# Performance work log

Measured on AMD Instinct MI355X. Metric: run time of the kernel, lower is better.

The kernel has to match this reference:

```python
import jax, jax.numpy as jnp
import numpy as np

D_MODEL = 2048
EXPAND = 2
D_INNER = EXPAND * D_MODEL      # 4096
HEADDIM = 64
NHEADS = D_INNER // HEADDIM     # 64
D_STATE = 128
NGROUPS = 1
D_CONV = 4
CHUNK = 256
CONV_DIM = D_INNER + 2 * NGROUPS * D_STATE          # 4352
D_IN_PROJ = 2 * D_INNER + 2 * NGROUPS * D_STATE + NHEADS  # 8512
EPS = 1e-5


def setup_inputs() -> dict:
    key = jax.random.key(0)
    ks = jax.random.split(key, 8)
    B, L = 2, 2048
    u = jax.random.normal(ks[0], (B, L, D_MODEL), jnp.float32)
    W_in = jax.random.normal(ks[1], (D_IN_PROJ, D_MODEL), jnp.float32) / np.sqrt(D_MODEL)
    conv_w = jax.random.normal(ks[2], (CONV_DIM, D_CONV), jnp.float32) * 0.2
    conv_b = jax.random.normal(ks[3], (CONV_DIM,), jnp.float32) * 0.05
    # dt_bias initialized exactly as in the torch module
    dt = jnp.exp(jax.random.uniform(ks[4], (NHEADS,)) * (np.log(0.1) - np.log(0.001)) + np.log(0.001))
    dt = jnp.clip(dt, 1e-4)
    dt_bias = dt + jnp.log(-jnp.expm1(-dt))
    A_log = jnp.log(jax.random.uniform(ks[5], (NHEADS,), minval=1.0, maxval=16.0))
    D = jnp.ones((NHEADS,), jnp.float32)
    norm_w = jnp.ones((D_INNER,), jnp.float32)
    W_out = jax.random.normal(ks[6], (D_MODEL, D_INNER), jnp.float32) / np.sqrt(D_INNER)
    return dict(u=u, W_in=W_in, conv_w=conv_w, conv_b=conv_b, dt_bias=dt_bias,
                A_log=A_log, D=D, norm_w=norm_w, W_out=W_out)


def _segsum(x):
    # x: (..., l) -> (..., l, l) with out[i, j] = sum_{k=j+1..i} x[k] (lower-tri, -inf above)
    cs = jnp.cumsum(x, -1)
    seg = cs[..., :, None] - cs[..., None, :]
    l = x.shape[-1]
    mask = jnp.tril(jnp.ones((l, l), bool))
    return jnp.where(mask, seg, -jnp.inf)


def reference(u, W_in, conv_w, conv_b, dt_bias, A_log, D, norm_w, W_out):
    B, L, _ = u.shape
    zxbcdt = u @ W_in.T                                   # (B, L, 8512)
    z, xBC, dt_raw = jnp.split(zxbcdt, [D_INNER, D_INNER + CONV_DIM], axis=-1)
    # depthwise causal conv1d + SiLU (padding = d_conv-1, truncated to seqlen)
    xpad = jnp.pad(xBC, ((0, 0), (D_CONV - 1, 0), (0, 0)))
    xconv = conv_b + sum(xpad[:, w:w + L, :] * conv_w[:, w] for w in range(D_CONV))
    xBC = jax.nn.silu(xconv)
    x, Bm, Cm = jnp.split(xBC, [D_INNER, D_INNER + NGROUPS * D_STATE], axis=-1)
    x = x.reshape(B, L, NHEADS, HEADDIM)
    hpg = NHEADS // NGROUPS
    Bh = jnp.repeat(Bm.reshape(B, L, NGROUPS, D_STATE), hpg, axis=2)  # (B,L,H,N)
    Ch = jnp.repeat(Cm.reshape(B, L, NGROUPS, D_STATE), hpg, axis=2)
    dt = jax.nn.softplus(dt_raw + dt_bias)                # (B, L, H)
    A = -jnp.exp(A_log)                                   # (H,)
    nchunks = L // CHUNK
    def chunk(t):
        return t.reshape(B, nchunks, CHUNK, *t.shape[2:])
    xc, Bc, Cc, dtc = chunk(x), chunk(Bh), chunk(Ch), chunk(dt)
    xd = xc * dtc[..., None]                              # (B,C,Lc,H,P)
    dA = jnp.transpose(dtc * A, (0, 3, 1, 2))             # (B,H,C,Lc)
    A_cum = jnp.cumsum(dA, -1)
    Lmat = jnp.exp(_segsum(dA))                           # (B,H,C,Lc,Lc) lower-tri decays
    # intra-chunk (diagonal blocks)
    Y_diag = jnp.einsum('bclhn,bcshn,bhcls,bcshp->bclhp', Cc, Bc, Lmat, xd)
    # chunk end-states
    decay_states = jnp.exp(A_cum[..., -1:] - A_cum)       # (B,H,C,Lc)
    states = jnp.einsum('bclhn,bhcl,bclhp->bchpn', Bc, decay_states, xd)
    # inter-chunk recurrence over chunk states
    chunk_sums = jnp.pad(A_cum[..., -1], ((0, 0), (0, 0), (1, 0)))  # (B,H,C+1)
    decay_chunk = jnp.exp(_segsum(chunk_sums))            # (B,H,C+1,C+1)
    states_pad = jnp.concatenate([jnp.zeros_like(states[:, :1]), states], axis=1)
    new_states = jnp.einsum('bhzc,bchpn->bzhpn', decay_chunk, states_pad)
    prev_states = new_states[:, :-1]                      # (B,C,H,P,N)
    Y_off = jnp.einsum('bclhn,bchpn,bhcl->bclhp', Cc, prev_states, jnp.exp(A_cum))
    y = (Y_diag + Y_off).reshape(B, L, NHEADS, HEADDIM)
    y = y + x * D[None, None, :, None]                    # per-head D skip
    y = y.reshape(B, L, D_INNER)
    # gated RMSNorm (norm_before_gate=False): rmsnorm(y * silu(z)) * w
    yg = y * jax.nn.silu(z)
    var = jnp.mean(yg * yg, axis=-1, keepdims=True)
    y = yg * jax.lax.rsqrt(var + EPS) * norm_w
    return y @ W_out.T                                    # (B, L, d_model)
```

## Files before the change

kernel.cpp:

```cpp
#include <hip/hip_runtime.h>

#define D_MODEL   2048
#define D_INNER   4096
#define HEADDIM   64
#define NHEADS    64
#define D_STATE   128
#define CHUNK     256
#define CONV_DIM  4352
#define D_IN_PROJ 8512
#define BATCH     2
#define SEQ       2048
#define NCHUNK    8
#define NROWS     4096
#define EPSV      1e-5f
#define CG        (CONV_DIM / 8)

typedef __attribute__((ext_vector_type(8))) short bf16x8;
typedef __attribute__((ext_vector_type(8))) unsigned short u16x8;
typedef __attribute__((ext_vector_type(4))) float f32x4;

#define AS1 __attribute__((address_space(1)))
#define AS3 __attribute__((address_space(3)))

#define BAR() do { asm volatile("" ::: "memory"); __builtin_amdgcn_s_barrier(); asm volatile("" ::: "memory"); } while (0)

__device__ __forceinline__ unsigned short f2bf(float f) {
  unsigned int x = __float_as_uint(f);
  unsigned int r = (x + 0x7fffu + ((x >> 16) & 1u)) >> 16;
  return (unsigned short)r;
}
__device__ __forceinline__ float bf2f(unsigned short u) {
  return __uint_as_float((unsigned int)u << 16);
}

__global__ void k_sentinel(float* out) { if (threadIdx.x == 0) out[0] = 1.0e6f; }

__global__ void k_f32_to_bf16_v4(const float* __restrict__ in, unsigned short* __restrict__ out, long n4) {
  long i = (long)blockIdx.x * blockDim.x + threadIdx.x;
  long stride = (long)gridDim.x * blockDim.x;
  for (; i < n4; i += stride) {
    float4 v = ((const float4*)in)[i];
    ushort4 o = make_ushort4(f2bf(v.x), f2bf(v.y), f2bf(v.z), f2bf(v.w));
    ((ushort4*)out)[i] = o;
  }
}

__global__ void k_usplit(const float* __restrict__ in, unsigned short* __restrict__ hi,
                         unsigned short* __restrict__ lo, long n4) {
  long i = (long)blockIdx.x * blockDim.x + threadIdx.x;
  long stride = (long)gridDim.x * blockDim.x;
  for (; i < n4; i += stride) {
    float4 v = ((const float4*)in)[i];
    ushort4 h, l;
    h.x = f2bf(v.x); l.x = f2bf(v.x - bf2f(h.x));
    h.y = f2bf(v.y); l.y = f2bf(v.y - bf2f(h.y));
    h.z = f2bf(v.z); l.z = f2bf(v.z - bf2f(h.z));
    h.w = f2bf(v.w); l.w = f2bf(v.w - bf2f(h.w));
    ((ushort4*)hi)[i] = h;
    ((ushort4*)lo)[i] = l;
  }
}

__global__ void k_wpack(const float* __restrict__ W, unsigned short* __restrict__ whl) {
  long i = (long)blockIdx.x * blockDim.x + threadIdx.x;
  if (i >= (long)64 * D_MODEL) return;
  float v = W[(size_t)8448 * D_MODEL + i];
  unsigned short h = f2bf(v);
  whl[i] = h;
  whl[(size_t)64 * D_MODEL + i] = f2bf(v - bf2f(h));
}

__global__ __launch_bounds__(256, 2) void k_dtm(const unsigned short* __restrict__ uhi,
                                                const unsigned short* __restrict__ ulo,
                                                const unsigned short* __restrict__ whl,
                                                float* __restrict__ PD) {
  __shared__ __align__(16) short lds[2][256 * 64];
  const int t = threadIdx.x;
  const int lane = t & 63;
  const int w = t >> 6;
  const int ks = (int)blockIdx.x & 3;
  const int m0 = ((int)blockIdx.x >> 2) * 64;
  const int kbase = ks * 512;

  f32x4 acc1[8], acc2[4];
#pragma unroll
  for (int j = 0; j < 8; ++j) { f32x4 z = {0.f, 0.f, 0.f, 0.f}; acc1[j] = z; }
#pragma unroll
  for (int j = 0; j < 4; ++j) { f32x4 z = {0.f, 0.f, 0.f, 0.f}; acc2[j] = z; }

  const int srow = t >> 3;
  const int schunk = (t & 7) ^ (srow & 7);
  const unsigned short* gU = uhi + (size_t)(m0 + srow) * D_MODEL + kbase + schunk * 8;
  const unsigned short* gL = ulo + (size_t)(m0 + srow) * D_MODEL + kbase + schunk * 8;
  const unsigned short* gW = whl + (size_t)srow * D_MODEL + kbase + schunk * 8;

  auto STAGE = [&](int buf, int kt) {
    char* d = (char*)&lds[buf][0] + t * 16;
#pragma unroll
    for (int ii = 0; ii < 2; ++ii)
      __builtin_amdgcn_global_load_lds((const AS1 void*)(gU + (size_t)ii * 32 * D_MODEL + (size_t)kt * 64),
                                       (AS3 void*)(d + ii * 4096), 16, 0, 0);
#pragma unroll
    for (int ii = 0; ii < 2; ++ii)
      __builtin_amdgcn_global_load_lds((const AS1 void*)(gL + (size_t)ii * 32 * D_MODEL + (size_t)kt * 64),
                                       (AS3 void*)(d + 8192 + ii * 4096), 16, 0, 0);
#pragma unroll
    for (int ii = 0; ii < 4; ++ii)
      __builtin_amdgcn_global_load_lds((const AS1 void*)(gW + (size_t)ii * 32 * D_MODEL + (size_t)kt * 64),
                                       (AS3 void*)(d + 16384 + ii * 4096), 16, 0, 0);
  };

  STAGE(0, 0);

  const int NT = 512 / 64;
  const int ar = w * 16 + (lane & 15);
  const int kof = (lane >> 4) * 8;
  const int rsw = (lane & 7) * 8;
  int cur = 0;
  for (int kt = 0; kt < NT; ++kt) {
    if (kt + 1 < NT) {
      STAGE(cur ^ 1, kt + 1);
      asm volatile("s_waitcnt vmcnt(8)" ::: "memory");
    } else {
      asm volatile("s_waitcnt vmcnt(0)" ::: "memory");
    }
    __builtin_amdgcn_s_barrier();
    asm volatile("" ::: "memory");
    const short* L = &lds[cur][0];
#pragma unroll
    for (int kk = 0; kk < 2; ++kk) {
      const int off = (kk * 32 + kof) ^ rsw;
      bf16x8 ah = *(const bf16x8*)(L + ar * 64 + off);
      bf16x8 al = *(const bf16x8*)(L + (64 + ar) * 64 + off);
#pragma unroll
      for (int j = 0; j < 8; ++j) {
        bf16x8 bj = *(const bf16x8*)(L + (128 + j * 16 + (lane & 15)) * 64 + off);
        acc1[j] = __builtin_amdgcn_mfma_f32_16x16x32_bf16(ah, bj, acc1[j], 0, 0, 0);
        if (j < 4) acc2[j] = __builtin_amdgcn_mfma_f32_16x16x32_bf16(al, bj, acc2[j], 0, 0, 0);
      }
    }
    asm volatile("" ::: "memory");
    __builtin_amdgcn_s_barrier();
    asm volatile("" ::: "memory");
    cur ^= 1;
  }

  const int crow = (lane >> 4) * 4;
  float* P = PD + (size_t)ks * BATCH * NHEADS * SEQ;
#pragma unroll
  for (int j = 0; j < 4; ++j) {
    int h = j * 16 + (lane & 15);
#pragma unroll
    for (int r = 0; r < 4; ++r) {
      int row = m0 + w * 16 + crow + r;
      float v = acc1[j][r] + acc1[j + 4][r] + acc2[j][r];
      P[(size_t)((row >> 11) * NHEADS + h) * SEQ + (row & 2047)] = v;
    }
  }
}

__global__ __launch_bounds__(256) void k_dtred(const float* __restrict__ PD, const float* __restrict__ dt_bias,
                                               const float* __restrict__ A_log,
                                               float* __restrict__ dt_t, float* __restrict__ A_cum) {
  const int bh = blockIdx.x;
  const int h = bh & 63;
  const int t = threadIdx.x;
  const float bias = dt_bias[h];
  const float A = -expf(A_log[h]);
  const size_t base = (size_t)bh * SEQ;
  const size_t pstride = (size_t)BATCH * NHEADS * SEQ;
  __shared__ float s[256];
  for (int c = 0; c < NCHUNK; ++c) {
    int l = c * CHUNK + t;
    float v = PD[base + l] + PD[pstride + base + l] + PD[2 * pstride + base + l] + PD[3 * pstride + base + l] + bias;
    float dtv = (v > 20.f) ? v : log1pf(expf(v));
    dt_t[base + l] = dtv;
    s[t] = dtv * A;
    __syncthreads();
    for (int off = 1; off < 256; off <<= 1) {
      float x = (t >= off) ? s[t - off] : 0.f;
      __syncthreads();
      s[t] += x;
      __syncthreads();
    }
    A_cum[((size_t)bh * NCHUNK + c) * CHUNK + t] = s[t];
    __syncthreads();
  }
}

__global__ __launch_bounds__(512, 2) void k_gemm8p(const unsigned short* __restrict__ A,
                                                   const unsigned short* __restrict__ B,
                                                   unsigned short* __restrict__ C, int M, int N, int K) {
  __shared__ __align__(16) short lds[2][32768];
  const int t = threadIdx.x;
  const int lane = t & 63;
  const int wid = t >> 6;
  const int wr = wid >> 2;
  const int wc = wid & 3;
  const int ntx = N / 256;
  const int nwg = (int)gridDim.x;
  const int bid = (int)blockIdx.x;
  const int swzb = (bid & 7) * (nwg >> 3) + (bid >> 3);
  const int m0 = (swzb / ntx) * 256;
  const int n0 = (swzb % ntx) * 256;

  f32x4 acc[8][4];
#pragma unroll
  for (int i = 0; i < 8; ++i)
#pragma unroll
    for (int j = 0; j < 4; ++j) { f32x4 z = {0.f, 0.f, 0.f, 0.f}; acc[i][j] = z; }

  const int srow = t >> 3;
  const int schunk = (t & 7) ^ (srow & 7);
  const unsigned short* gA = A + (size_t)(m0 + srow) * K + schunk * 8;
  const unsigned short* gB = B + (size_t)(n0 + srow) * K + schunk * 8;

  auto STAGE_HALF = [&](int buf, int kt, int which) {
    const unsigned short* g = (which < 2 ? gA : gB) + (size_t)(which & 1) * 128 * K + (size_t)kt * 64;
    char* d = (char*)lds + buf * 65536 + which * 16384 + t * 16;
    __builtin_amdgcn_global_load_lds((const AS1 void*)g, (AS3 void*)d, 16, 0, 0);
    __builtin_amdgcn_global_load_lds((const AS1 void*)(g + (size_t)64 * K), (AS3 void*)(d + 8192), 16, 0, 0);
  };

  const int NT = K / 64;
  STAGE_HALF(0, 0, 0); STAGE_HALF(0, 0, 1); STAGE_HALF(0, 0, 2); STAGE_HALF(0, 0, 3);
  STAGE_HALF(1, 1, 2); STAGE_HALF(1, 1, 0); STAGE_HALF(1, 1, 1);
  asm volatile("s_waitcnt vmcnt(6)" ::: "memory");
  BAR();

  const int ar = wr * 128 + (lane & 15);
  const int br = wc * 64 + (lane & 15);
  const int kof = (lane >> 4) * 8;
  const int rsw = (lane & 7) * 8;

  for (int kt = 0; kt < NT; ++kt) {
    const int buf = kt & 1;
    const short* As = &lds[buf][0];
    const short* Bs = &lds[buf][16384];
    const bool s1 = (kt + 1 < NT);
    const bool s2 = (kt + 2 < NT);
    bf16x8 aLo[4][2], aHi[4][2], bLo[2][2], bHi[2][2];

#pragma unroll
    for (int i = 0; i < 4; ++i)
#pragma unroll
      for (int k = 0; k < 2; ++k) aLo[i][k] = *(const bf16x8*)(As + (ar + i * 16) * 64 + ((k * 32 + kof) ^ rsw));
#pragma unroll
    for (int j = 0; j < 2; ++j)
#pragma unroll
      for (int k = 0; k < 2; ++k) bLo[j][k] = *(const bf16x8*)(Bs + (br + j * 16) * 64 + ((k * 32 + kof) ^ rsw));
    if (s1) STAGE_HALF(buf ^ 1, kt + 1, 3);
    BAR();
    __builtin_amdgcn_s_setprio(1);
#pragma unroll
    for (int k = 0; k < 2; ++k)
#pragma unroll
      for (int i = 0; i < 4; ++i)
#pragma unroll
        for (int j = 0; j < 2; ++j)
          acc[i][j] = __builtin_amdgcn_mfma_f32_16x16x32_bf16(aLo[i][k], bLo[j][k], acc[i][j], 0, 0, 0);
    __builtin_amdgcn_s_setprio(0);
    BAR();

#pragma unroll
    for (int j = 0; j < 2; ++j)
#pragma unroll
      for (int k = 0; k < 2; ++k) bHi[j][k] = *(const bf16x8*)(Bs + (br + (j + 2) * 16) * 64 + ((k * 32 + kof) ^ rsw));
    BAR();
    __builtin_amdgcn_s_setprio(1);
#pragma unroll
    for (int k = 0; k < 2; ++k)
#pragma unroll
      for (int i = 0; i < 4; ++i)
#pragma unroll
        for (int j = 0; j < 2; ++j)
          acc[i][j + 2] = __builtin_amdgcn_mfma_f32_16x16x32_bf16(aLo[i][k], bHi[j][k], acc[i][j + 2], 0, 0, 0);
    __builtin_amdgcn_s_setprio(0);
    BAR();

#pragma unroll
    for (int i = 0; i < 4; ++i)
#pragma unroll
      for (int k = 0; k < 2; ++k) aHi[i][k] = *(const bf16x8*)(As + (ar + (i + 4) * 16) * 64 + ((k * 32 + kof) ^ rsw));
    if (s2) STAGE_HALF(buf, kt + 2, 2);
    BAR();
    __builtin_amdgcn_s_setprio(1);
#pragma unroll
    for (int k = 0; k < 2; ++k)
#pragma unroll
      for (int i = 0; i < 4; ++i)
#pragma unroll
        for (int j = 0; j < 2; ++j)
          acc[i + 4][j] = __builtin_amdgcn_mfma_f32_16x16x32_bf16(aHi[i][k], bLo[j][k], acc[i + 4][j], 0, 0, 0);
    __builtin_amdgcn_s_setprio(0);
    BAR();

    if (s2) { STAGE_HALF(buf, kt + 2, 0); STAGE_HALF(buf, kt + 2, 1); }
    if (s2) { asm volatile("s_waitcnt vmcnt(6)" ::: "memory"); }
    else    { asm volatile("s_waitcnt vmcnt(0)" ::: "memory"); }
    BAR();
    __builtin_amdgcn_s_setprio(1);
#pragma unroll
    for (int k = 0; k < 2; ++k)
#pragma unroll
      for (int i = 0; i < 4; ++i)
#pragma unroll
        for (int j = 0; j < 2; ++j)
          acc[i + 4][j + 2] = __builtin_amdgcn_mfma_f32_16x16x32_bf16(aHi[i][k], bHi[j][k], acc[i + 4][j + 2], 0, 0, 0);
    __builtin_amdgcn_s_setprio(0);
    BAR();
  }

  const int crow = (lane >> 4) * 4;
  const int ccol = lane & 15;
#pragma unroll
  for (int i = 0; i < 8; ++i)
#pragma unroll
    for (int j = 0; j < 4; ++j) {
      size_t base = (size_t)(m0 + wr * 128 + i * 16 + crow) * N + (n0 + wc * 64 + j * 16 + ccol);
#pragma unroll
      for (int r = 0; r < 4; ++r) C[base + (size_t)r * N] = f2bf(acc[i][j][r]);
    }
}

template <int BF16OUT>
__global__ __launch_bounds__(256, 2) void k_gemm128(const unsigned short* __restrict__ A,
                                                    const unsigned short* __restrict__ B,
                                                    void* __restrict__ Cv, int M, int N, int K) {
  constexpr int BK = 64;
  __shared__ __align__(16) short lds[2][256 * BK];
  const int t = threadIdx.x;
  const int lane = t & 63;
  const int wid = t >> 6;
  const int wr = wid >> 1;
  const int wc = wid & 1;
  const int ntx = N / 128;
  const int nwg = (int)gridDim.x;
  const int bid = (int)blockIdx.x;
  const int swzb = (bid & 7) * (nwg >> 3) + (bid >> 3);
  const int m0 = (swzb / ntx) * 128;
  const int n0 = (swzb % ntx) * 128;

  f32x4 acc[4][4];
#pragma unroll
  for (int i = 0; i < 4; ++i)
#pragma unroll
    for (int j = 0; j < 4; ++j) { f32x4 z = {0.f, 0.f, 0.f, 0.f}; acc[i][j] = z; }

  const int srow = t >> 3;
  const int schunk = (t & 7) ^ (srow & 7);
  const unsigned short* gA = A + (size_t)(m0 + srow) * K + schunk * 8;
  const unsigned short* gB = B + (size_t)(n0 + srow) * K + schunk * 8;

  auto STAGE = [&](int buf, int kt) {
    char* dA = (char*)&lds[buf][0] + t * 16;
    char* dB = (char*)&lds[buf][128 * BK] + t * 16;
#pragma unroll
    for (int ii = 0; ii < 4; ++ii)
      __builtin_amdgcn_global_load_lds((const AS1 void*)(gA + (size_t)ii * 32 * K + kt * BK),
                                       (AS3 void*)(dA + ii * 4096), 16, 0, 0);
#pragma unroll
    for (int ii = 0; ii < 4; ++ii)
      __builtin_amdgcn_global_load_lds((const AS1 void*)(gB + (size_t)ii * 32 * K + kt * BK),
                                       (AS3 void*)(dB + ii * 4096), 16, 0, 0);
  };

  STAGE(0, 0);

  const int NT = K / BK;
  const int ar = wr * 64 + (lane & 15);
  const int br = wc * 64 + (lane & 15);
  const int kof = (lane >> 4) * 8;
  const int rsw = (lane & 7) * 8;
  int cur = 0;
  for (int kt = 0; kt < NT; ++kt) {
    if (kt + 1 < NT) {
      STAGE(cur ^ 1, kt + 1);
      asm volatile("s_waitcnt vmcnt(8)" ::: "memory");
    } else {
      asm volatile("s_waitcnt vmcnt(0)" ::: "memory");
    }
    __builtin_amdgcn_s_barrier();
    asm volatile("" ::: "memory");
    const short* As = &lds[cur][0];
    const short* Bs = &lds[cur][128 * BK];
#pragma unroll
    for (int kk = 0; kk < 2; ++kk) {
      bf16x8 bfr[4];
#pragma unroll
      for (int j = 0; j < 4; ++j)
        bfr[j] = *(const bf16x8*)(Bs + (br + j * 16) * BK + ((kk * 32 + kof) ^ rsw));
#pragma unroll
      for (int i = 0; i < 4; ++i) {
        bf16x8 af = *(const bf16x8*)(As + (ar + i * 16) * BK + ((kk * 32 + kof) ^ rsw));
#pragma unroll
        for (int j = 0; j < 4; ++j)
          acc[i][j] = __builtin_amdgcn_mfma_f32_16x16x32_bf16(af, bfr[j], acc[i][j], 0, 0, 0);
      }
    }
    asm volatile("" ::: "memory");
    __builtin_amdgcn_s_barrier();
    asm volatile("" ::: "memory");
    cur ^= 1;
  }

  const int crow = (lane >> 4) * 4;
  const int ccol = lane & 15;
#pragma unroll
  for (int i = 0; i < 4; ++i)
#pragma unroll
    for (int j = 0; j < 4; ++j) {
      size_t base = (size_t)(m0 + wr * 64 + i * 16 + crow) * N + (n0 + wc * 64 + j * 16 + ccol);
      if (BF16OUT) {
        unsigned short* C = (unsigned short*)Cv;
#pragma unroll
        for (int r = 0; r < 4; ++r) C[base + (size_t)r * N] = f2bf(acc[i][j][r]);
      } else {
        float* C = (float*)Cv;
#pragma unroll
        for (int r = 0; r < 4; ++r) C[base + (size_t)r * N] = acc[i][j][r];
      }
    }
}

__global__ void k_conv_pack(const float* __restrict__ cw, const float* __restrict__ cb,
                            unsigned short* __restrict__ wT, unsigned short* __restrict__ bT) {
  int i = blockIdx.x * blockDim.x + threadIdx.x;
  if (i < CONV_DIM) {
#pragma unroll
    for (int w = 0; w < 4; ++w) wT[w * CONV_DIM + i] = f2bf(cw[i * 4 + w]);
    bT[i] = f2bf(cb[i]);
  }
}

__global__ __launch_bounds__(256) void k_conv_silu(const unsigned short* __restrict__ xb,
                                                   const unsigned short* __restrict__ wT,
                                                   const unsigned short* __restrict__ bT,
                                                   unsigned short* __restrict__ out) {
  long idx = (long)blockIdx.x * blockDim.x + threadIdx.x;
  if (idx >= (long)(NROWS / 4) * CG) return;
  int c8 = (int)(idx % CG);
  long rq = idx / CG;
  int l0 = (int)((rq & (SEQ / 4 - 1)) * 4);
  long brow = (rq >> 9) * (long)SEQ;
  int ch0 = c8 * 8;

  u16x8 wv[4];
#pragma unroll
  for (int w = 0; w < 4; ++w) wv[w] = *(const u16x8*)(wT + w * CONV_DIM + ch0);
  u16x8 bv = *(const u16x8*)(bT + ch0);

  u16x8 xr[7];
#pragma unroll
  for (int i = 0; i < 7; ++i) {
    int ls = l0 - 3 + i;
    if (ls >= 0) xr[i] = *(const u16x8*)(xb + (brow + ls) * (long)CONV_DIM + ch0);
    else { u16x8 z = {0, 0, 0, 0, 0, 0, 0, 0}; xr[i] = z; }
  }

#pragma unroll
  for (int r = 0; r < 4; ++r) {
    float acc[8];
#pragma unroll
    for (int e = 0; e < 8; ++e) acc[e] = bf2f(bv[e]);
#pragma unroll
    for (int w = 0; w < 4; ++w)
#pragma unroll
      for (int e = 0; e < 8; ++e) acc[e] += bf2f(xr[r + w][e]) * bf2f(wv[w][e]);
    u16x8 o;
#pragma unroll
    for (int e = 0; e < 8; ++e) o[e] = f2bf(acc[e] / (1.f + expf(-acc[e])));
    *(u16x8*)(out + (brow + l0 + r) * (long)CONV_DIM + ch0) = o;
  }
}

__global__ __launch_bounds__(256) void k_cbtt(const unsigned short* __restrict__ xbc, unsigned short* __restrict__ cbt_t) {
  const int bid = blockIdx.x;
  const int sp = bid & 3;
  const int bc = bid >> 2;
  const int b = bc >> 3, c = bc & 7;
  const int t = threadIdx.x;
  const int lane = t & 63;
  const int w = t >> 6;
  const int g = lane >> 4;
  __shared__ unsigned short Cs[256][72];
  __shared__ unsigned short Bs2[64][72];
  const long rowbase = (long)b * SEQ + c * CHUNK;
  f32x4 acc[4][4];
#pragma unroll
  for (int i = 0; i < 4; ++i)
#pragma unroll
    for (int j = 0; j < 4; ++j) { f32x4 z = {0.f, 0.f, 0.f, 0.f}; acc[i][j] = z; }

  for (int np = 0; np < 2; ++np) {
    __syncthreads();
    for (int i = t; i < 256 * 16; i += 256) {
      int row = i >> 4, c4 = (i & 15) * 4;
      ushort4 v = *(const ushort4*)(xbc + (rowbase + row) * (long)CONV_DIM + D_INNER + D_STATE + np * 64 + c4);
      *(ushort4*)&Cs[row][c4] = v;
    }
    for (int i = t; i < 64 * 16; i += 256) {
      int row = i >> 4, c4 = (i & 15) * 4;
      ushort4 v = *(const ushort4*)(xbc + (rowbase + sp * 64 + row) * (long)CONV_DIM + D_INNER + np * 64 + c4);
      *(ushort4*)&Bs2[row][c4] = v;
    }
    __syncthreads();
#pragma unroll
    for (int ks = 0; ks < 2; ++ks) {
      const int kofs = ks * 32 + g * 8;
      bf16x8 af[4], bfr[4];
#pragma unroll
      for (int i = 0; i < 4; ++i) af[i] = *(const bf16x8*)&Cs[w * 64 + i * 16 + (lane & 15)][kofs];
#pragma unroll
      for (int j = 0; j < 4; ++j) bfr[j] = *(const bf16x8*)&Bs2[j * 16 + (lane & 15)][kofs];
#pragma unroll
      for (int i = 0; i < 4; ++i)
#pragma unroll
        for (int j = 0; j < 4; ++j)
          acc[i][j] = __builtin_amdgcn_mfma_f32_16x16x32_bf16(af[i], bfr[j], acc[i][j], 0, 0, 0);
    }
  }
  unsigned short* ob = cbt_t + (long)bc * CHUNK * CHUNK;
#pragma unroll
  for (int i = 0; i < 4; ++i)
#pragma unroll
    for (int j = 0; j < 4; ++j) {
      int l0 = w * 64 + i * 16 + g * 4;
      int s = sp * 64 + j * 16 + (lane & 15);
#pragma unroll
      for (int r = 0; r < 4; ++r) ob[(long)(l0 + r) * CHUNK + s] = f2bf(acc[i][j][r]);
    }
}

__global__ __launch_bounds__(256) void k_states(const unsigned short* __restrict__ xbc, const float* __restrict__ dt_t,
                                                const float* __restrict__ A_cum, float* __restrict__ states) {
  const int bid = blockIdx.x;
  const int h = bid & 63;
  const int bc = bid >> 6;
  const int b = bc >> 3, c = bc & 7;
  const int t = threadIdx.x;
  const int lane = t & 63;
  const int w = t >> 6;
  const int g = lane >> 4;
  __shared__ unsigned short BT[128][72];
  __shared__ unsigned short WXT[64][72];
  __shared__ float csL[256], dtL[256];
  const long rowbase = (long)b * SEQ + c * CHUNK;
  const long bh8 = ((long)(b * NHEADS + h)) * NCHUNK + c;
  const float* acum = A_cum + bh8 * CHUNK;
  if (t < 256) { csL[t] = acum[t]; dtL[t] = dt_t[((size_t)(b * NHEADS + h)) * SEQ + c * CHUNK + t]; }
  float cs_last = acum[255];
  f32x4 acc[2][4];
#pragma unroll
  for (int i = 0; i < 2; ++i)
#pragma unroll
    for (int j = 0; j < 4; ++j) { f32x4 z = {0.f, 0.f, 0.f, 0.f}; acc[i][j] = z; }

  for (int lp = 0; lp < 4; ++lp) {
    __syncthreads();
    for (int i = t; i < 64 * 32; i += 256) {
      int l = i >> 5, n4 = (i & 31) * 4;
      ushort4 v = *(const ushort4*)(xbc + (rowbase + lp * 64 + l) * (long)CONV_DIM + D_INNER + n4);
      BT[n4 + 0][l] = v.x; BT[n4 + 1][l] = v.y; BT[n4 + 2][l] = v.z; BT[n4 + 3][l] = v.w;
    }
    for (int i = t; i < 64 * 16; i += 256) {
      int l = i >> 4, p4 = (i & 15) * 4;
      int lg = lp * 64 + l;
      float wgt = expf(cs_last - csL[lg]) * dtL[lg];
      ushort4 v = *(const ushort4*)(xbc + (rowbase + lg) * (long)CONV_DIM + h * HEADDIM + p4);
      WXT[p4 + 0][l] = f2bf(bf2f(v.x) * wgt);
      WXT[p4 + 1][l] = f2bf(bf2f(v.y) * wgt);
      WXT[p4 + 2][l] = f2bf(bf2f(v.z) * wgt);
      WXT[p4 + 3][l] = f2bf(bf2f(v.w) * wgt);
    }
    __syncthreads();
#pragma unroll
    for (int ks = 0; ks < 2; ++ks) {
      const int kofs = ks * 32 + g * 8;
      bf16x8 am[2], bp[4];
#pragma unroll
      for (int i = 0; i < 2; ++i) am[i] = *(const bf16x8*)&BT[w * 32 + i * 16 + (lane & 15)][kofs];
#pragma unroll
      for (int j = 0; j < 4; ++j) bp[j] = *(const bf16x8*)&WXT[j * 16 + (lane & 15)][kofs];
#pragma unroll
      for (int i = 0; i < 2; ++i)
#pragma unroll
        for (int j = 0; j < 4; ++j)
          acc[i][j] = __builtin_amdgcn_mfma_f32_16x16x32_bf16(am[i], bp[j], acc[i][j], 0, 0, 0);
    }
  }
  float* sp = states + ((long)bc * NHEADS + h) * (D_STATE * HEADDIM);
#pragma unroll
  for (int i = 0; i < 2; ++i)
#pragma unroll
    for (int j = 0; j < 4; ++j) {
      int n0 = w * 32 + i * 16 + g * 4;
      int p = j * 16 + (lane & 15);
#pragma unroll
      for (int r = 0; r < 4; ++r) sp[(long)(n0 + r) * HEADDIM + p] = acc[i][j][r];
    }
}

__global__ void k_scan(const float* __restrict__ states, const float* __restrict__ A_cum, unsigned short* __restrict__ psb) {
  long idx = (long)blockIdx.x * blockDim.x + threadIdx.x;
  if (idx >= (long)BATCH * NHEADS * D_STATE * HEADDIM) return;
  int p = idx & 63;
  int n = (int)((idx >> 6) & 127);
  long bh = idx >> 13;
  int h = (int)(bh & 63);
  int b = (int)(bh >> 6);
  float S = 0.f;
  for (int c = 0; c < NCHUNK; ++c) {
    long soff = (((long)(b * NCHUNK + c) * NHEADS + h) * (D_STATE * HEADDIM)) + (long)n * HEADDIM + p;
    psb[soff] = f2bf(S);
    float decay = expf(A_cum[(bh * NCHUNK + c) * CHUNK + 255]);
    S = S * decay + states[soff];
  }
}

__global__ __launch_bounds__(256) void k_y(const unsigned short* __restrict__ xbc, const float* __restrict__ dt_t,
                                           const float* __restrict__ A_cum, const unsigned short* __restrict__ cbt_t,
                                           const unsigned short* __restrict__ psb, const float* __restrict__ Dp,
                                           unsigned short* __restrict__ y) {
  const int bid = blockIdx.x;
  const int h = bid & 63;
  const int bc = bid >> 6;
  const int b = bc >> 3, c = bc & 7;
  const int t = threadIdx.x;
  const int lane = t & 63;
  const int w = t >> 6;
  const int g = lane >> 4;
  __shared__ unsigned short Abuf[256][72];
  __shared__ unsigned short Bbuf[64][72];
  __shared__ float csL[256], dtL[256], expL[256];
  const long rowbase = (long)b * SEQ + c * CHUNK;
  const long bh8 = ((long)(b * NHEADS + h)) * NCHUNK + c;
  const float* acum = A_cum + bh8 * CHUNK;
  if (t < 256) {
    float cv = acum[t];
    csL[t] = cv;
    expL[t] = expf(cv);
    dtL[t] = dt_t[((size_t)(b * NHEADS + h)) * SEQ + c * CHUNK + t];
  }
  f32x4 acc[4][4];
#pragma unroll
  for (int i = 0; i < 4; ++i)
#pragma unroll
    for (int j = 0; j < 4; ++j) { f32x4 z = {0.f, 0.f, 0.f, 0.f}; acc[i][j] = z; }

  const unsigned short* psbase = psb + ((long)bc * NHEADS + h) * (D_STATE * HEADDIM);
  for (int np = 0; np < 2; ++np) {
    __syncthreads();
    for (int i = t; i < 256 * 16; i += 256) {
      int row = i >> 4, c4 = (i & 15) * 4;
      float el = expL[row];
      ushort4 v = *(const ushort4*)(xbc + (rowbase + row) * (long)CONV_DIM + D_INNER + D_STATE + np * 64 + c4);
      ushort4 o = make_ushort4(f2bf(bf2f(v.x) * el), f2bf(bf2f(v.y) * el), f2bf(bf2f(v.z) * el), f2bf(bf2f(v.w) * el));
      *(ushort4*)&Abuf[row][c4] = o;
    }
    for (int i = t; i < 64 * 16; i += 256) {
      int n = i >> 4, p4 = (i & 15) * 4;
      ushort4 v = *(const ushort4*)(psbase + (long)(np * 64 + n) * HEADDIM + p4);
      Bbuf[p4 + 0][n] = v.x; Bbuf[p4 + 1][n] = v.y; Bbuf[p4 + 2][n] = v.z; Bbuf[p4 + 3][n] = v.w;
    }
    __syncthreads();
#pragma unroll
    for (int ks = 0; ks < 2; ++ks) {
      const int kofs = ks * 32 + g * 8;
      bf16x8 af[4], bfr[4];
#pragma unroll
      for (int i = 0; i < 4; ++i) af[i] = *(const bf16x8*)&Abuf[w * 64 + i * 16 + (lane & 15)][kofs];
#pragma unroll
      for (int j = 0; j < 4; ++j) bfr[j] = *(const bf16x8*)&Bbuf[j * 16 + (lane & 15)][kofs];
#pragma unroll
      for (int i = 0; i < 4; ++i)
#pragma unroll
        for (int j = 0; j < 4; ++j)
          acc[i][j] = __builtin_amdgcn_mfma_f32_16x16x32_bf16(af[i], bfr[j], acc[i][j], 0, 0, 0);
    }
  }

  const unsigned short* cbtb = cbt_t + (long)bc * CHUNK * CHUNK;
  for (int sp = 0; sp < 4; ++sp) {
    __syncthreads();
    for (int i = t; i < 64 * 8; i += 256) {
      int s = i >> 3, p0 = (i & 7) * 8;
      u16x8 v = *(const u16x8*)(xbc + (rowbase + sp * 64 + s) * (long)CONV_DIM + h * HEADDIM + p0);
#pragma unroll
      for (int e = 0; e < 8; ++e) Bbuf[p0 + e][s] = v[e];
    }
    __syncthreads();
    if (sp > w) continue;
#pragma unroll
    for (int ks = 0; ks < 2; ++ks) {
      const int kofs = ks * 32 + g * 8;
      bf16x8 bfr[4];
#pragma unroll
      for (int j = 0; j < 4; ++j) bfr[j] = *(const bf16x8*)&Bbuf[j * 16 + (lane & 15)][kofs];
      const int sbase = sp * 64 + ks * 32 + g * 8;
#pragma unroll
      for (int i = 0; i < 4; ++i) {
        if (sp == w && ks * 32 > i * 16 + 15) continue;
        const int l = w * 64 + i * 16 + (lane & 15);
        u16x8 cv = *(const u16x8*)(cbtb + (long)l * CHUNK + sbase);
        const float cl = csL[l];
        bf16x8 af;
#pragma unroll
        for (int e = 0; e < 8; ++e) {
          int s = sbase + e;
          float val = (s <= l) ? bf2f(cv[e]) * expf(cl - csL[s]) * dtL[s] : 0.f;
          af[e] = (short)f2bf(val);
        }
#pragma unroll
        for (int j = 0; j < 4; ++j)
          acc[i][j] = __builtin_amdgcn_mfma_f32_16x16x32_bf16(af, bfr[j], acc[i][j], 0, 0, 0);
      }
    }
  }

  const float Dh = Dp[h];
#pragma unroll
  for (int i = 0; i < 4; ++i) {
    int l0 = w * 64 + i * 16 + g * 4;
#pragma unroll
    for (int r = 0; r < 4; ++r) {
      long grow = rowbase + l0 + r;
      const unsigned short* xrow = xbc + grow * (long)CONV_DIM + h * HEADDIM;
      unsigned short* yrow = y + grow * (long)D_INNER + h * HEADDIM;
#pragma unroll
      for (int j = 0; j < 4; ++j) {
        int p = j * 16 + (lane & 15);
        yrow[p] = f2bf(acc[i][j][r] + bf2f(xrow[p]) * Dh);
      }
    }
  }
}

__global__ __launch_bounds__(256) void k_norm(unsigned short* yz, const unsigned short* __restrict__ zb,
                                              const float* __restrict__ norm_w, unsigned short* out) {
  const int row = blockIdx.x;
  const int t = threadIdx.x;
  const unsigned short* yr = yz + (size_t)row * D_INNER;
  const unsigned short* zr = zb + (size_t)row * D_INNER;
  float yv[16];
  float ss = 0.f;
#pragma unroll
  for (int j = 0; j < 4; ++j) {
    int e = (t + j * 256) * 4;
    ushort4 yy = *(const ushort4*)(yr + e);
    ushort4 zz = *(const ushort4*)(zr + e);
    float z0 = bf2f(zz.x), z1 = bf2f(zz.y), z2 = bf2f(zz.z), z3 = bf2f(zz.w);
    float g0 = bf2f(yy.x) * z0 / (1.f + expf(-z0));
    float g1 = bf2f(yy.y) * z1 / (1.f + expf(-z1));
    float g2 = bf2f(yy.z) * z2 / (1.f + expf(-z2));
    float g3 = bf2f(yy.w) * z3 / (1.f + expf(-z3));
    ss += g0 * g0 + g1 * g1 + g2 * g2 + g3 * g3;
    yv[j * 4 + 0] = g0; yv[j * 4 + 1] = g1; yv[j * 4 + 2] = g2; yv[j * 4 + 3] = g3;
  }
#pragma unroll
  for (int off = 32; off > 0; off >>= 1) ss += __shfl_xor(ss, off);
  __shared__ float red[4];
  if ((t & 63) == 0) red[t >> 6] = ss;
  __syncthreads();
  float tot = red[0] + red[1] + red[2] + red[3];
  float scale = rsqrtf(tot / (float)D_INNER + EPSV);
  unsigned short* orow = out + (size_t)row * D_INNER;
#pragma unroll
  for (int j = 0; j < 4; ++j) {
    int e = (t + j * 256) * 4;
    float4 w = *(const float4*)(norm_w + e);
    ushort4 o = make_ushort4(f2bf(yv[j * 4 + 0] * scale * w.x), f2bf(yv[j * 4 + 1] * scale * w.y),
                             f2bf(yv[j * 4 + 2] * scale * w.z), f2bf(yv[j * 4 + 3] * scale * w.w));
    *(ushort4*)(orow + e) = o;
  }
}

extern "C" void kernel_launch(void* const* d_in, const int* in_sizes, int n_in,
                              void* d_out, int out_size, void* d_ws, size_t ws_size,
                              hipStream_t stream) {
  const float* u       = (const float*)d_in[0];
  const float* W_in    = (const float*)d_in[1];
  const float* conv_w  = (const float*)d_in[2];
  const float* conv_b  = (const float*)d_in[3];
  const float* dt_bias = (const float*)d_in[4];
  const float* A_log   = (const float*)d_in[5];
  const float* Dp      = (const float*)d_in[6];
  const float* norm_w  = (const float*)d_in[7];
  const float* W_out   = (const float*)d_in[8];
  float* out = (float*)d_out;

  char* ws = (char*)d_ws;
  size_t off = 0;
  auto alloc = [&](size_t bytes) { char* p = ws + off; off += (bytes + 255) & ~(size_t)255; return p; };
  unsigned short* ub   = (unsigned short*)alloc((size_t)NROWS * D_MODEL * 2);
  unsigned short* winb = (unsigned short*)alloc((size_t)D_IN_PROJ * D_MODEL * 2);
  unsigned short* zb   = (unsigned short*)alloc((size_t)NROWS * D_INNER * 2);
  unsigned short* xb   = (unsigned short*)alloc((size_t)NROWS * CONV_DIM * 2);
  unsigned short* xbcb = (unsigned short*)alloc((size_t)NROWS * CONV_DIM * 2);
  float* dtt  = (float*)alloc((size_t)BATCH * NHEADS * SEQ * 4);
  float* acum = (float*)alloc((size_t)BATCH * NHEADS * NCHUNK * CHUNK * 4);
  unsigned short* cwT = (unsigned short*)alloc((size_t)4 * CONV_DIM * 2);
  unsigned short* cbT = (unsigned short*)alloc((size_t)CONV_DIM * 2);
  unsigned short* whl = (unsigned short*)alloc((size_t)128 * D_MODEL * 2);
  float* PD = (float*)alloc((size_t)4 * BATCH * NHEADS * SEQ * 4);
  unsigned short* wob = ub;
  unsigned short* cbt = winb;
  unsigned short* psb = winb + (size_t)BATCH * NCHUNK * CHUNK * CHUNK + 1024;
  unsigned short* ulob = xbcb;
  unsigned short* yb = xb;
  float* states = (float*)d_out;

  if (off > ws_size) {
    k_sentinel<<<1, 64, 0, stream>>>(out);
    return;
  }

  k_usplit<<<2048, 256, 0, stream>>>(u, ub, ulob, (long)NROWS * D_MODEL / 4);
  k_f32_to_bf16_v4<<<2048, 256, 0, stream>>>(W_in, winb, (long)D_IN_PROJ * D_MODEL / 4);
  k_wpack<<<(64 * D_MODEL + 255) / 256, 256, 0, stream>>>(W_in, whl);
  k_conv_pack<<<(CONV_DIM + 255) / 256, 256, 0, stream>>>(conv_w, conv_b, cwT, cbT);
  k_gemm8p<<<(NROWS / 256) * (D_INNER / 256), 512, 0, stream>>>(ub, winb, zb, NROWS, D_INNER, D_MODEL);
  k_gemm128<1><<<(NROWS / 128) * (CONV_DIM / 128), 256, 0, stream>>>(ub, winb + (size_t)D_INNER * D_MODEL, xb, NROWS, CONV_DIM, D_MODEL);
  k_dtm<<<256, 256, 0, stream>>>(ub, ulob, whl, PD);
  k_dtred<<<BATCH * NHEADS, 256, 0, stream>>>(PD, dt_bias, A_log, dtt, acum);
  k_conv_silu<<<(int)(((long)(NROWS / 4) * CG + 255) / 256), 256, 0, stream>>>(xb, cwT, cbT, xbcb);
  k_cbtt<<<BATCH * NCHUNK * 4, 256, 0, stream>>>(xbcb, cbt);
  k_states<<<BATCH * NCHUNK * NHEADS, 256, 0, stream>>>(xbcb, dtt, acum, states);
  k_scan<<<(BATCH * NHEADS * D_STATE * HEADDIM + 255) / 256, 256, 0, stream>>>(states, acum, psb);
  k_y<<<BATCH * NCHUNK * NHEADS, 256, 0, stream>>>(xbcb, dtt, acum, cbt, psb, Dp, yb);
  k_norm<<<NROWS, 256, 0, stream>>>(yb, zb, norm_w, yb);
  k_f32_to_bf16_v4<<<2048, 256, 0, stream>>>(W_out, wob, (long)D_MODEL * D_INNER / 4);
  k_gemm128<0><<<(NROWS / 128) * (D_MODEL / 128), 256, 0, stream>>>(yb, wob, out, NROWS, D_MODEL, D_INNER);
}
```

Measured before the change: 499.9 us.

## Fuse preprocessing kernels into one launch and group-swizzle GEMM tile order

Merges the four input/weight conversion kernels (u hi/lo split, W_in bf16 cast, dt-weight hi/lo pack, conv weight pack) into a single launch that dispatches on block ID ranges. This removes three kernel launches and their tail gaps. Separately, both GEMMs now map blocks to tiles in groups of 8 M-tiles sweeping across N, rather than row-major, to improve L2 reuse of A and B tiles. The grouped mapping assumes the M tile count divides evenly by 8, which holds for these shapes.

```diff
diff --git a/kernel.cpp b/kernel.cpp
--- a/kernel.cpp
+++ b/kernel.cpp
@@ -35,6 +35,47 @@
 
 __global__ void k_sentinel(float* out) { if (threadIdx.x == 0) out[0] = 1.0e6f; }
 
+__global__ void k_prep(const float* __restrict__ u, unsigned short* __restrict__ uhi, unsigned short* __restrict__ ulo,
+                       const float* __restrict__ W, unsigned short* __restrict__ winb, unsigned short* __restrict__ whl,
+                       const float* __restrict__ cw, const float* __restrict__ cb,
+                       unsigned short* __restrict__ cwT, unsigned short* __restrict__ cbT) {
+  const int b = blockIdx.x;
+  const int t = threadIdx.x;
+  if (b < 2048) {
+    const long n4 = (long)NROWS * D_MODEL / 4;
+    for (long i = (long)b * 256 + t; i < n4; i += 2048L * 256) {
+      float4 v = ((const float4*)u)[i];
+      ushort4 h, l;
+      h.x = f2bf(v.x); l.x = f2bf(v.x - bf2f(h.x));
+      h.y = f2bf(v.y); l.y = f2bf(v.y - bf2f(h.y));
+      h.z = f2bf(v.z); l.z = f2bf(v.z - bf2f(h.z));
+      h.w = f2bf(v.w); l.w = f2bf(v.w - bf2f(h.w));
+      ((ushort4*)uhi)[i] = h;
+      ((ushort4*)ulo)[i] = l;
+    }
+  } else if (b < 6144) {
+    const long n4 = (long)D_IN_PROJ * D_MODEL / 4;
+    for (long i = (long)(b - 2048) * 256 + t; i < n4; i += 4096L * 256) {
+      float4 v = ((const float4*)W)[i];
+      ushort4 o = make_ushort4(f2bf(v.x), f2bf(v.y), f2bf(v.z), f2bf(v.w));
+      ((ushort4*)winb)[i] = o;
+    }
+  } else if (b < 6656) {
+    long i = (long)(b - 6144) * 256 + t;
+    float v = W[(size_t)8448 * D_MODEL + i];
+    unsigned short h = f2bf(v);
+    whl[i] = h;
+    whl[(size_t)64 * D_MODEL + i] = f2bf(v - bf2f(h));
+  } else {
+    int i = (b - 6656) * 256 + t;
+    if (i < CONV_DIM) {
+#pragma unroll
+      for (int w = 0; w < 4; ++w) cwT[w * CONV_DIM + i] = f2bf(cw[i * 4 + w]);
+      cbT[i] = f2bf(cb[i]);
+    }
+  }
+}
+
 __global__ void k_f32_to_bf16_v4(const float* __restrict__ in, unsigned short* __restrict__ out, long n4) {
   long i = (long)blockIdx.x * blockDim.x + threadIdx.x;
   long stride = (long)gridDim.x * blockDim.x;
@@ -43,31 +84,6 @@
     ushort4 o = make_ushort4(f2bf(v.x), f2bf(v.y), f2bf(v.z), f2bf(v.w));
     ((ushort4*)out)[i] = o;
   }
-}
-
-__global__ void k_usplit(const float* __restrict__ in, unsigned short* __restrict__ hi,
-                         unsigned short* __restrict__ lo, long n4) {
-  long i = (long)blockIdx.x * blockDim.x + threadIdx.x;
-  long stride = (long)gridDim.x * blockDim.x;
-  for (; i < n4; i += stride) {
-    float4 v = ((const float4*)in)[i];
-    ushort4 h, l;
-    h.x = f2bf(v.x); l.x = f2bf(v.x - bf2f(h.x));
-    h.y = f2bf(v.y); l.y = f2bf(v.y - bf2f(h.y));
-    h.z = f2bf(v.z); l.z = f2bf(v.z - bf2f(h.z));
-    h.w = f2bf(v.w); l.w = f2bf(v.w - bf2f(h.w));
-    ((ushort4*)hi)[i] = h;
-    ((ushort4*)lo)[i] = l;
-  }
-}
-
-__global__ void k_wpack(const float* __restrict__ W, unsigned short* __restrict__ whl) {
-  long i = (long)blockIdx.x * blockDim.x + threadIdx.x;
-  if (i >= (long)64 * D_MODEL) return;
-  float v = W[(size_t)8448 * D_MODEL + i];
-  unsigned short h = f2bf(v);
-  whl[i] = h;
-  whl[(size_t)64 * D_MODEL + i] = f2bf(v - bf2f(h));
 }
 
 __global__ __launch_bounds__(256, 2) void k_dtm(const unsigned short* __restrict__ uhi,
@@ -200,9 +216,12 @@
   const int ntx = N / 256;
   const int nwg = (int)gridDim.x;
   const int bid = (int)blockIdx.x;
-  const int swzb = (bid & 7) * (nwg >> 3) + (bid >> 3);
-  const int m0 = (swzb / ntx) * 256;
-  const int n0 = (swzb % ntx) * 256;
+  const int swz = (bid & 7) * (nwg >> 3) + (bid >> 3);
+  const int grp = ntx << 3;
+  const int gid = swz / grp;
+  const int rem = swz - gid * grp;
+  const int m0 = ((gid << 3) + (rem & 7)) * 256;
+  const int n0 = (rem >> 3) * 256;
 
   f32x4 acc[8][4];
 #pragma unroll
@@ -337,9 +356,12 @@
   const int ntx = N / 128;
   const int nwg = (int)gridDim.x;
   const int bid = (int)blockIdx.x;
-  const int swzb = (bid & 7) * (nwg >> 3) + (bid >> 3);
-  const int m0 = (swzb / ntx) * 128;
-  const int n0 = (swzb % ntx) * 128;
+  const int swz = (bid & 7) * (nwg >> 3) + (bid >> 3);
+  const int grp = ntx << 3;
+  const int gid = swz / grp;
+  const int rem = swz - gid * grp;
+  const int m0 = ((gid << 3) + (rem & 7)) * 128;
+  const int n0 = (rem >> 3) * 128;
 
   f32x4 acc[4][4];
 #pragma unroll
@@ -421,16 +443,6 @@
         for (int r = 0; r < 4; ++r) C[base + (size_t)r * N] = acc[i][j][r];
       }
     }
-}
-
-__global__ void k_conv_pack(const float* __restrict__ cw, const float* __restrict__ cb,
-                            unsigned short* __restrict__ wT, unsigned short* __restrict__ bT) {
-  int i = blockIdx.x * blockDim.x + threadIdx.x;
-  if (i < CONV_DIM) {
-#pragma unroll
-    for (int w = 0; w < 4; ++w) wT[w * CONV_DIM + i] = f2bf(cw[i * 4 + w]);
-    bT[i] = f2bf(cb[i]);
-  }
 }
 
 __global__ __launch_bounds__(256) void k_conv_silu(const unsigned short* __restrict__ xb,
@@ -815,10 +827,7 @@
     return;
   }
 
-  k_usplit<<<2048, 256, 0, stream>>>(u, ub, ulob, (long)NROWS * D_MODEL / 4);
-  k_f32_to_bf16_v4<<<2048, 256, 0, stream>>>(W_in, winb, (long)D_IN_PROJ * D_MODEL / 4);
-  k_wpack<<<(64 * D_MODEL + 255) / 256, 256, 0, stream>>>(W_in, whl);
-  k_conv_pack<<<(CONV_DIM + 255) / 256, 256, 0, stream>>>(conv_w, conv_b, cwT, cbT);
+  k_prep<<<6673, 256, 0, stream>>>(u, ub, ulob, W_in, winb, whl, conv_w, conv_b, cwT, cbT);
   k_gemm8p<<<(NROWS / 256) * (D_INNER / 256), 512, 0, stream>>>(ub, winb, zb, NROWS, D_INNER, D_MODEL);
   k_gemm128<1><<<(NROWS / 128) * (CONV_DIM / 128), 256, 0, stream>>>(ub, winb + (size_t)D_INNER * D_MODEL, xb, NROWS, CONV_DIM, D_MODEL);
   k_dtm<<<256, 256, 0, stream>>>(ub, ulob, whl, PD);
```

Result: faster. 478.5 us (-4.3%).
